# Performance work log

Measured on AMD Instinct MI355X. Metric: run time of the kernel, lower is better.

The kernel has to match this reference:

```python
import jax, jax.numpy as jnp
import numpy as np

B, C, H, W = 32, 256, 32, 32
C8 = C // 8


def setup_inputs() -> dict:
    key = jax.random.key(0)
    ks = jax.random.split(key, 8)
    s = 1.0 / np.sqrt(C)
    return {
        "x": jax.random.normal(ks[0], (B, C, H, W), dtype=jnp.float32),
        "Wq": jax.random.normal(ks[1], (C8, C), dtype=jnp.float32) * s,
        "bq": jax.random.normal(ks[2], (C8,), dtype=jnp.float32) * s,
        "Wk": jax.random.normal(ks[3], (C8, C), dtype=jnp.float32) * s,
        "bk": jax.random.normal(ks[4], (C8,), dtype=jnp.float32) * s,
        "Wv": jax.random.normal(ks[5], (C, C), dtype=jnp.float32) * s,
        "bv": jax.random.normal(ks[6], (C,), dtype=jnp.float32) * s,
        "gamma": jax.random.normal(ks[7], (1,), dtype=jnp.float32) * 0.1,
    }


def reference(x, Wq, bq, Wk, bk, Wv, bv, gamma):
    b, c, h, w = x.shape
    n = h * w
    xf = x.reshape(b, c, n)  # [B, C, N]
    # 1x1 convs == per-pixel linear projections
    q = jnp.einsum('dc,bcn->bnd', Wq, xf) + bq            # [B, N, C/8]
    k = jnp.einsum('dc,bcn->bdn', Wk, xf) + bk[:, None]    # [B, C/8, N]
    v = jnp.einsum('dc,bcn->bdn', Wv, xf) + bv[:, None]    # [B, C, N]
    energy = jnp.einsum('bnd,bdm->bnm', q, k)              # [B, N, N], no scaling (as in source)
    attn = jax.nn.softmax(energy, axis=-1)                 # softmax over keys
    # out[:, :, i] = sum_j V[:, :, j] * attn[i, j]
    out = jnp.einsum('bdn,bmn->bdm', v, attn)              # [B, C, N]
    out = out.reshape(b, c, h, w)
    return gamma * out + x
```

## Files before the change

kernel.cpp:

```cpp
#include <hip/hip_runtime.h>
#include <math.h>

#define BB 32
#define CC 256
#define CQ 32
#define NN 1024

typedef short bf16x8 __attribute__((ext_vector_type(8)));
typedef float f32x4  __attribute__((ext_vector_type(4)));
typedef unsigned short u16;

__device__ __forceinline__ u16 f2bf(float f) {
    unsigned u = __float_as_uint(f);
    u = (u + 0x7FFFu + ((u >> 16) & 1u)) >> 16;
    return (u16)u;
}

__global__ void wpack_kernel(const float* __restrict__ Wq,
                             const float* __restrict__ Wk,
                             const float* __restrict__ Wv,
                             u16* __restrict__ wfrag)
{
    const int o = blockIdx.x * 256 + threadIdx.x;
    const int j    = o & 7;
    const int lane = (o >> 3) & 63;
    const int kc   = (o >> 9) & 7;
    const int rt   = o >> 12;
    const int row  = rt * 16 + (lane & 15);
    const int col  = kc * 32 + (lane >> 4) * 8 + j;
    const float v = (row < 32) ? Wq[row * 256 + col]
                  : (row < 64) ? Wk[(row - 32) * 256 + col]
                               : Wv[(row - 64) * 256 + col];
    wfrag[o] = f2bf(v);
}

struct QSmem {
    union {
        u16 xs[64][272];
        u16 osv[CC][72];
    };
    u16 osqk[64][72];
};

__global__ __launch_bounds__(256, 2) void qkv_kernel(
    const float* __restrict__ x, const u16* __restrict__ wfrag,
    const float* __restrict__ bq, const float* __restrict__ bk,
    const float* __restrict__ bv,
    u16* __restrict__ qt, u16* __restrict__ kt, u16* __restrict__ vv)
{
    __shared__ QSmem sm;
    const int b = blockIdx.y, n0 = blockIdx.x * 64;
    const int t = threadIdx.x;
    const int lane = t & 63, w = t >> 6;
    const int quad = lane >> 4, c16 = lane & 15;

    {
        const float* xb = x + (size_t)b * CC * NN + n0;
        const int cg = t >> 4;
        const int n4 = (t & 15) * 4;
        float4 f[16];
#pragma unroll
        for (int it = 0; it < 16; ++it)
            f[it] = *(const float4*)(xb + (size_t)(it * 16 + cg) * NN + n4);
#pragma unroll
        for (int it = 0; it < 16; ++it) {
            const int c = it * 16 + cg;
            sm.xs[n4 + 0][c] = f2bf(f[it].x);
            sm.xs[n4 + 1][c] = f2bf(f[it].y);
            sm.xs[n4 + 2][c] = f2bf(f[it].z);
            sm.xs[n4 + 3][c] = f2bf(f[it].w);
        }
    }
    __syncthreads();

    f32x4 acc[5][4];
#pragma unroll
    for (int i = 0; i < 5; ++i)
#pragma unroll
        for (int j = 0; j < 4; ++j) acc[i][j] = (f32x4){0.f, 0.f, 0.f, 0.f};

#pragma unroll 2
    for (int k = 0; k < 8; ++k) {
        const int c0 = k * 32;
        bf16x8 wa[5], xb[4];
#pragma unroll
        for (int rs = 0; rs < 5; ++rs)
            wa[rs] = *(const bf16x8*)&wfrag[(size_t)(((w * 5 + rs) * 8 + k) * 64 + lane) * 8];
#pragma unroll
        for (int ns = 0; ns < 4; ++ns)
            xb[ns] = *(const bf16x8*)&sm.xs[ns * 16 + c16][c0 + quad * 8];
#pragma unroll
        for (int rs = 0; rs < 5; ++rs)
#pragma unroll
            for (int ns = 0; ns < 4; ++ns)
                acc[rs][ns] = __builtin_amdgcn_mfma_f32_16x16x32_bf16(
                    wa[rs], xb[ns], acc[rs][ns], 0, 0, 0);
    }

    __syncthreads();

#pragma unroll
    for (int rs = 0; rs < 5; ++rs) {
#pragma unroll
        for (int r = 0; r < 4; ++r) {
            const int rg = w * 80 + rs * 16 + quad * 4 + r;
            const float bias = (rg < 32) ? bq[rg] : (rg < 64) ? bk[rg - 32] : bv[rg - 64];
#pragma unroll
            for (int ns = 0; ns < 4; ++ns) {
                const int n = ns * 16 + c16;
                const u16 h = f2bf(acc[rs][ns][r] + bias);
                if (rg < 64) sm.osqk[n][rg] = h;
                else         sm.osv[rg - 64][n] = h;
            }
        }
    }
    __syncthreads();

    {
        u16* dst = (w >= 2) ? kt : qt;
        const int dof = (w >= 2) ? 32 : 0;
        const int wl = w & 1;
        const size_t base = ((size_t)b * NN + n0) * CQ;
#pragma unroll
        for (int it = 0; it < 4; ++it) {
            const int o = wl * 2048 + it * 512 + lane * 8;
            const int n = o >> 5, d = o & 31;
            const bf16x8 v = *(const bf16x8*)&sm.osqk[n][d + dof];
            *(bf16x8*)&dst[base + o] = v;
        }
    }
#pragma unroll
    for (int it = 0; it < 8; ++it) {
        const int o = it * 2048 + t * 8;
        const int c = o >> 6, n = o & 63;
        const bf16x8 v = *(const bf16x8*)&sm.osv[c][n];
        *(bf16x8*)&vv[((size_t)b * CC + c) * NN + n0 + n] = v;
    }
}

__global__ __launch_bounds__(256, 2) void attn_kernel(
    const u16* __restrict__ qt, const u16* __restrict__ kt,
    const u16* __restrict__ vv, const float* __restrict__ x,
    const float* __restrict__ gamma_p, float* __restrict__ out)
{
    __shared__ float ps[2][64][68];

    const int bid  = blockIdx.x;
    const int xcd  = bid & 7;
    const int slot = bid >> 3;
    const int b    = (xcd << 2) | (slot >> 4);
    const int m0   = (slot & 15) * 64;

    const int t = threadIdx.x, lane = t & 63, w = t >> 6;
    const int quad = lane >> 4, c16 = lane & 15;

    const bf16x8 qa = *(const bf16x8*)&qt[((size_t)b * NN + m0 + w * 16 + c16) * CQ + quad * 8];

    bf16x8 ones;
#pragma unroll
    for (int j = 0; j < 8; ++j) ones[j] = (short)0x3F80;

    f32x4 accO[4][4];
    f32x4 lsum[4];
#pragma unroll
    for (int i = 0; i < 4; ++i) {
        lsum[i] = (f32x4){0.f, 0.f, 0.f, 0.f};
#pragma unroll
        for (int j = 0; j < 4; ++j) accO[i][j] = (f32x4){0.f, 0.f, 0.f, 0.f};
    }

    const u16* vbase = vv + (size_t)b * CC * NN;
    const u16* kbase = kt + (size_t)b * NN * CQ;

    bf16x8 kb[4];
#pragma unroll
    for (int s = 0; s < 4; ++s)
        kb[s] = *(const bf16x8*)&kbase[(size_t)(s * 16 + c16) * CQ + quad * 8];

    for (int step = 0; step < 16; ++step) {
        const int nbase = step * 64;
        float* psb = &ps[step & 1][0][0];

        bf16x8 va[4][2];
#pragma unroll
        for (int cs = 0; cs < 4; ++cs)
#pragma unroll
            for (int kc = 0; kc < 2; ++kc)
                va[cs][kc] = *(const bf16x8*)&vbase[
                    (size_t)(w * 64 + cs * 16 + c16) * NN + nbase + kc * 32 + quad * 8];

        f32x4 accS[4];
#pragma unroll
        for (int s = 0; s < 4; ++s)
            accS[s] = __builtin_amdgcn_mfma_f32_16x16x32_bf16(
                qa, kb[s], (f32x4){0.f, 0.f, 0.f, 0.f}, 0, 0, 0);

#pragma unroll
        for (int r = 0; r < 4; ++r)
#pragma unroll
            for (int s = 0; s < 4; ++s)
                psb[(w * 16 + quad * 4 + r) * 68 + s * 16 + c16] = __expf(accS[s][r]);

        if (step < 15) {
#pragma unroll
            for (int s = 0; s < 4; ++s)
                kb[s] = *(const bf16x8*)&kbase[(size_t)(nbase + 64 + s * 16 + c16) * CQ + quad * 8];
        }

        __syncthreads();

#pragma unroll
        for (int ms = 0; ms < 4; ++ms) {
            bf16x8 pb[2];
#pragma unroll
            for (int kc = 0; kc < 2; ++kc) {
                const f32x4 p0 = *(const f32x4*)&psb[(ms * 16 + c16) * 68 + kc * 32 + quad * 8];
                const f32x4 p1 = *(const f32x4*)&psb[(ms * 16 + c16) * 68 + kc * 32 + quad * 8 + 4];
                bf16x8 pk;
                pk[0] = (short)f2bf(p0[0]); pk[1] = (short)f2bf(p0[1]);
                pk[2] = (short)f2bf(p0[2]); pk[3] = (short)f2bf(p0[3]);
                pk[4] = (short)f2bf(p1[0]); pk[5] = (short)f2bf(p1[1]);
                pk[6] = (short)f2bf(p1[2]); pk[7] = (short)f2bf(p1[3]);
                pb[kc] = pk;
            }
            lsum[ms] = __builtin_amdgcn_mfma_f32_16x16x32_bf16(ones, pb[0], lsum[ms], 0, 0, 0);
            lsum[ms] = __builtin_amdgcn_mfma_f32_16x16x32_bf16(ones, pb[1], lsum[ms], 0, 0, 0);
#pragma unroll
            for (int cs = 0; cs < 4; ++cs) {
#pragma unroll
                for (int kc = 0; kc < 2; ++kc)
                    accO[cs][ms] = __builtin_amdgcn_mfma_f32_16x16x32_bf16(
                        va[cs][kc], pb[kc], accO[cs][ms], 0, 0, 0);
            }
        }
    }

    const float gamma = gamma_p[0];
#pragma unroll
    for (int ms = 0; ms < 4; ++ms) {
        const float inv = gamma / lsum[ms][0];
        const int m = m0 + ms * 16 + c16;
#pragma unroll
        for (int cs = 0; cs < 4; ++cs) {
            const int cbase = w * 64 + cs * 16 + quad * 4;
#pragma unroll
            for (int r = 0; r < 4; ++r) {
                const size_t idx = ((size_t)b * CC + cbase + r) * NN + m;
                out[idx] = accO[cs][ms][r] * inv + x[idx];
            }
        }
    }
}

extern "C" void kernel_launch(void* const* d_in, const int* in_sizes, int n_in,
                              void* d_out, int out_size, void* d_ws, size_t ws_size,
                              hipStream_t stream)
{
    const float* x  = (const float*)d_in[0];
    const float* Wq = (const float*)d_in[1];
    const float* bq = (const float*)d_in[2];
    const float* Wk = (const float*)d_in[3];
    const float* bk = (const float*)d_in[4];
    const float* Wv = (const float*)d_in[5];
    const float* bv = (const float*)d_in[6];
    const float* gm = (const float*)d_in[7];
    float* out = (float*)d_out;

    u16* qt    = (u16*)d_ws;
    u16* kt    = qt + (size_t)BB * NN * CQ;
    u16* vv    = kt + (size_t)BB * NN * CQ;
    u16* wfrag = vv + (size_t)BB * CC * NN;

    wpack_kernel<<<320, 256, 0, stream>>>(Wq, Wk, Wv, wfrag);
    dim3 grid(16, BB);
    qkv_kernel<<<grid, 256, 0, stream>>>(x, wfrag, bq, bk, bv, qt, kt, vv);
    attn_kernel<<<512, 256, 0, stream>>>(qt, kt, vv, x, gm, out);
}
```

Measured before the change: 154.1 us.

## Halve query/pixel tile to 32 and double grids with XCD-aware mapping

Both the QKV projection and attention kernels now process 32 pixels/queries per block instead of 64, doubling the grid to 1024 blocks with an XCD-aware batch mapping and launch bounds raised to 4 blocks per CU. In attention, each step now covers 128 keys: wave pairs split the score computation across two 64-key halves, then the PV accumulation is done in two 64-key sub-steps, with V reloaded in between. The aim is more parallelism and occupancy on the many CUs. The cost is that V and K tiles are re-read from global memory twice as often per output, since reuse per block is halved.

```diff
diff --git a/kernel.cpp b/kernel.cpp
--- a/kernel.cpp
+++ b/kernel.cpp
@@ -36,35 +36,40 @@
 
 struct QSmem {
     union {
-        u16 xs[64][272];
-        u16 osv[CC][72];
+        u16 xs[32][272];
+        u16 osv[CC][40];
     };
-    u16 osqk[64][72];
+    u16 osqk[32][72];
 };
 
-__global__ __launch_bounds__(256, 2) void qkv_kernel(
+__global__ __launch_bounds__(256, 4) void qkv_kernel(
     const float* __restrict__ x, const u16* __restrict__ wfrag,
     const float* __restrict__ bq, const float* __restrict__ bk,
     const float* __restrict__ bv,
     u16* __restrict__ qt, u16* __restrict__ kt, u16* __restrict__ vv)
 {
     __shared__ QSmem sm;
-    const int b = blockIdx.y, n0 = blockIdx.x * 64;
+    const int bid  = blockIdx.x;
+    const int xcd  = bid & 7;
+    const int slot = bid >> 3;
+    const int b    = (xcd << 2) | (slot >> 5);
+    const int n0   = (slot & 31) * 32;
+
     const int t = threadIdx.x;
     const int lane = t & 63, w = t >> 6;
     const int quad = lane >> 4, c16 = lane & 15;
 
     {
         const float* xb = x + (size_t)b * CC * NN + n0;
-        const int cg = t >> 4;
-        const int n4 = (t & 15) * 4;
-        float4 f[16];
-#pragma unroll
-        for (int it = 0; it < 16; ++it)
-            f[it] = *(const float4*)(xb + (size_t)(it * 16 + cg) * NN + n4);
-#pragma unroll
-        for (int it = 0; it < 16; ++it) {
-            const int c = it * 16 + cg;
+        const int cr = t >> 3;
+        const int n4 = (t & 7) * 4;
+        float4 f[8];
+#pragma unroll
+        for (int it = 0; it < 8; ++it)
+            f[it] = *(const float4*)(xb + (size_t)(cr + 32 * it) * NN + n4);
+#pragma unroll
+        for (int it = 0; it < 8; ++it) {
+            const int c = cr + 32 * it;
             sm.xs[n4 + 0][c] = f2bf(f[it].x);
             sm.xs[n4 + 1][c] = f2bf(f[it].y);
             sm.xs[n4 + 2][c] = f2bf(f[it].z);
@@ -73,26 +78,26 @@
     }
     __syncthreads();
 
-    f32x4 acc[5][4];
+    f32x4 acc[5][2];
 #pragma unroll
     for (int i = 0; i < 5; ++i)
 #pragma unroll
-        for (int j = 0; j < 4; ++j) acc[i][j] = (f32x4){0.f, 0.f, 0.f, 0.f};
+        for (int j = 0; j < 2; ++j) acc[i][j] = (f32x4){0.f, 0.f, 0.f, 0.f};
 
 #pragma unroll 2
     for (int k = 0; k < 8; ++k) {
         const int c0 = k * 32;
-        bf16x8 wa[5], xb[4];
+        bf16x8 wa[5], xb[2];
 #pragma unroll
         for (int rs = 0; rs < 5; ++rs)
             wa[rs] = *(const bf16x8*)&wfrag[(size_t)(((w * 5 + rs) * 8 + k) * 64 + lane) * 8];
 #pragma unroll
-        for (int ns = 0; ns < 4; ++ns)
+        for (int ns = 0; ns < 2; ++ns)
             xb[ns] = *(const bf16x8*)&sm.xs[ns * 16 + c16][c0 + quad * 8];
 #pragma unroll
         for (int rs = 0; rs < 5; ++rs)
 #pragma unroll
-            for (int ns = 0; ns < 4; ++ns)
+            for (int ns = 0; ns < 2; ++ns)
                 acc[rs][ns] = __builtin_amdgcn_mfma_f32_16x16x32_bf16(
                     wa[rs], xb[ns], acc[rs][ns], 0, 0, 0);
     }
@@ -106,7 +111,7 @@
             const int rg = w * 80 + rs * 16 + quad * 4 + r;
             const float bias = (rg < 32) ? bq[rg] : (rg < 64) ? bk[rg - 32] : bv[rg - 64];
 #pragma unroll
-            for (int ns = 0; ns < 4; ++ns) {
+            for (int ns = 0; ns < 2; ++ns) {
                 const int n = ns * 16 + c16;
                 const u16 h = f2bf(acc[rs][ns][r] + bias);
                 if (rg < 64) sm.osqk[n][rg] = h;
@@ -119,55 +124,53 @@
     {
         u16* dst = (w >= 2) ? kt : qt;
         const int dof = (w >= 2) ? 32 : 0;
-        const int wl = w & 1;
         const size_t base = ((size_t)b * NN + n0) * CQ;
-#pragma unroll
-        for (int it = 0; it < 4; ++it) {
-            const int o = wl * 2048 + it * 512 + lane * 8;
-            const int n = o >> 5, d = o & 31;
-            const bf16x8 v = *(const bf16x8*)&sm.osqk[n][d + dof];
-            *(bf16x8*)&dst[base + o] = v;
-        }
-    }
-#pragma unroll
-    for (int it = 0; it < 8; ++it) {
+        const int o = (w & 1) * 512 + lane * 8;
+        const int n = o >> 5, d = o & 31;
+        const bf16x8 v = *(const bf16x8*)&sm.osqk[n][d + dof];
+        *(bf16x8*)&dst[base + o] = v;
+    }
+#pragma unroll
+    for (int it = 0; it < 4; ++it) {
         const int o = it * 2048 + t * 8;
-        const int c = o >> 6, n = o & 63;
+        const int c = o >> 5, n = o & 31;
         const bf16x8 v = *(const bf16x8*)&sm.osv[c][n];
         *(bf16x8*)&vv[((size_t)b * CC + c) * NN + n0 + n] = v;
     }
 }
 
-__global__ __launch_bounds__(256, 2) void attn_kernel(
+__global__ __launch_bounds__(256, 4) void attn_kernel(
     const u16* __restrict__ qt, const u16* __restrict__ kt,
     const u16* __restrict__ vv, const float* __restrict__ x,
     const float* __restrict__ gamma_p, float* __restrict__ out)
 {
-    __shared__ float ps[2][64][68];
+    __shared__ float ps[2][32][132];
 
     const int bid  = blockIdx.x;
     const int xcd  = bid & 7;
     const int slot = bid >> 3;
-    const int b    = (xcd << 2) | (slot >> 4);
-    const int m0   = (slot & 15) * 64;
+    const int b    = (xcd << 2) | (slot >> 5);
+    const int m0   = (slot & 31) * 32;
 
     const int t = threadIdx.x, lane = t & 63, w = t >> 6;
     const int quad = lane >> 4, c16 = lane & 15;
-
-    const bf16x8 qa = *(const bf16x8*)&qt[((size_t)b * NN + m0 + w * 16 + c16) * CQ + quad * 8];
+    const int mh = (w & 1) * 16;
+    const int nh = (w >> 1) * 64;
+
+    const bf16x8 qa = *(const bf16x8*)&qt[((size_t)b * NN + m0 + mh + c16) * CQ + quad * 8];
 
     bf16x8 ones;
 #pragma unroll
     for (int j = 0; j < 8; ++j) ones[j] = (short)0x3F80;
 
-    f32x4 accO[4][4];
-    f32x4 lsum[4];
-#pragma unroll
-    for (int i = 0; i < 4; ++i) {
-        lsum[i] = (f32x4){0.f, 0.f, 0.f, 0.f};
-#pragma unroll
-        for (int j = 0; j < 4; ++j) accO[i][j] = (f32x4){0.f, 0.f, 0.f, 0.f};
-    }
+    f32x4 accO[4][2];
+    f32x4 lsum[2];
+#pragma unroll
+    for (int i = 0; i < 4; ++i)
+#pragma unroll
+        for (int j = 0; j < 2; ++j) accO[i][j] = (f32x4){0.f, 0.f, 0.f, 0.f};
+    lsum[0] = (f32x4){0.f, 0.f, 0.f, 0.f};
+    lsum[1] = (f32x4){0.f, 0.f, 0.f, 0.f};
 
     const u16* vbase = vv + (size_t)b * CC * NN;
     const u16* kbase = kt + (size_t)b * NN * CQ;
@@ -175,10 +178,10 @@
     bf16x8 kb[4];
 #pragma unroll
     for (int s = 0; s < 4; ++s)
-        kb[s] = *(const bf16x8*)&kbase[(size_t)(s * 16 + c16) * CQ + quad * 8];
-
-    for (int step = 0; step < 16; ++step) {
-        const int nbase = step * 64;
+        kb[s] = *(const bf16x8*)&kbase[(size_t)(nh + s * 16 + c16) * CQ + quad * 8];
+
+    for (int step = 0; step < 8; ++step) {
+        const int nbase = step * 128;
         float* psb = &ps[step & 1][0][0];
 
         bf16x8 va[4][2];
@@ -199,23 +202,23 @@
         for (int r = 0; r < 4; ++r)
 #pragma unroll
             for (int s = 0; s < 4; ++s)
-                psb[(w * 16 + quad * 4 + r) * 68 + s * 16 + c16] = __expf(accS[s][r]);
-
-        if (step < 15) {
+                psb[(mh + quad * 4 + r) * 132 + nh + s * 16 + c16] = __expf(accS[s][r]);
+
+        if (step < 7) {
 #pragma unroll
             for (int s = 0; s < 4; ++s)
-                kb[s] = *(const bf16x8*)&kbase[(size_t)(nbase + 64 + s * 16 + c16) * CQ + quad * 8];
+                kb[s] = *(const bf16x8*)&kbase[(size_t)(nbase + 128 + nh + s * 16 + c16) * CQ + quad * 8];
         }
 
         __syncthreads();
 
 #pragma unroll
-        for (int ms = 0; ms < 4; ++ms) {
+        for (int ms = 0; ms < 2; ++ms) {
             bf16x8 pb[2];
 #pragma unroll
             for (int kc = 0; kc < 2; ++kc) {
-                const f32x4 p0 = *(const f32x4*)&psb[(ms * 16 + c16) * 68 + kc * 32 + quad * 8];
-                const f32x4 p1 = *(const f32x4*)&psb[(ms * 16 + c16) * 68 + kc * 32 + quad * 8 + 4];
+                const f32x4 p0 = *(const f32x4*)&psb[(ms * 16 + c16) * 132 + kc * 32 + quad * 8];
+                const f32x4 p1 = *(const f32x4*)&psb[(ms * 16 + c16) * 132 + kc * 32 + quad * 8 + 4];
                 bf16x8 pk;
                 pk[0] = (short)f2bf(p0[0]); pk[1] = (short)f2bf(p0[1]);
                 pk[2] = (short)f2bf(p0[2]); pk[3] = (short)f2bf(p0[3]);
@@ -226,18 +229,48 @@
             lsum[ms] = __builtin_amdgcn_mfma_f32_16x16x32_bf16(ones, pb[0], lsum[ms], 0, 0, 0);
             lsum[ms] = __builtin_amdgcn_mfma_f32_16x16x32_bf16(ones, pb[1], lsum[ms], 0, 0, 0);
 #pragma unroll
-            for (int cs = 0; cs < 4; ++cs) {
+            for (int cs = 0; cs < 4; ++cs)
 #pragma unroll
                 for (int kc = 0; kc < 2; ++kc)
                     accO[cs][ms] = __builtin_amdgcn_mfma_f32_16x16x32_bf16(
                         va[cs][kc], pb[kc], accO[cs][ms], 0, 0, 0);
+        }
+
+#pragma unroll
+        for (int cs = 0; cs < 4; ++cs)
+#pragma unroll
+            for (int kc = 0; kc < 2; ++kc)
+                va[cs][kc] = *(const bf16x8*)&vbase[
+                    (size_t)(w * 64 + cs * 16 + c16) * NN + nbase + 64 + kc * 32 + quad * 8];
+
+#pragma unroll
+        for (int ms = 0; ms < 2; ++ms) {
+            bf16x8 pb[2];
+#pragma unroll
+            for (int kc = 0; kc < 2; ++kc) {
+                const f32x4 p0 = *(const f32x4*)&psb[(ms * 16 + c16) * 132 + 64 + kc * 32 + quad * 8];
+                const f32x4 p1 = *(const f32x4*)&psb[(ms * 16 + c16) * 132 + 64 + kc * 32 + quad * 8 + 4];
+                bf16x8 pk;
+                pk[0] = (short)f2bf(p0[0]); pk[1] = (short)f2bf(p0[1]);
+                pk[2] = (short)f2bf(p0[2]); pk[3] = (short)f2bf(p0[3]);
+                pk[4] = (short)f2bf(p1[0]); pk[5] = (short)f2bf(p1[1]);
+                pk[6] = (short)f2bf(p1[2]); pk[7] = (short)f2bf(p1[3]);
+                pb[kc] = pk;
             }
+            lsum[ms] = __builtin_amdgcn_mfma_f32_16x16x32_bf16(ones, pb[0], lsum[ms], 0, 0, 0);
+            lsum[ms] = __builtin_amdgcn_mfma_f32_16x16x32_bf16(ones, pb[1], lsum[ms], 0, 0, 0);
+#pragma unroll
+            for (int cs = 0; cs < 4; ++cs)
+#pragma unroll
+                for (int kc = 0; kc < 2; ++kc)
+                    accO[cs][ms] = __builtin_amdgcn_mfma_f32_16x16x32_bf16(
+                        va[cs][kc], pb[kc], accO[cs][ms], 0, 0, 0);
         }
     }
 
     const float gamma = gamma_p[0];
 #pragma unroll
-    for (int ms = 0; ms < 4; ++ms) {
+    for (int ms = 0; ms < 2; ++ms) {
         const float inv = gamma / lsum[ms][0];
         const int m = m0 + ms * 16 + c16;
 #pragma unroll
@@ -272,7 +305,6 @@
     u16* wfrag = vv + (size_t)BB * CC * NN;
 
     wpack_kernel<<<320, 256, 0, stream>>>(Wq, Wk, Wv, wfrag);
-    dim3 grid(16, BB);
-    qkv_kernel<<<grid, 256, 0, stream>>>(x, wfrag, bq, bk, bv, qt, kt, vv);
-    attn_kernel<<<512, 256, 0, stream>>>(qt, kt, vv, x, gm, out);
-}
+    qkv_kernel<<<1024, 256, 0, stream>>>(x, wfrag, bq, bk, bv, qt, kt, vv);
+    attn_kernel<<<1024, 256, 0, stream>>>(qt, kt, vv, x, gm, out);
+}
```

Result: slower. 194.5 us (+26.2%).
